# Optimization experiments

Measured on AMD Instinct MI355X. Metric: run time of the kernel, lower is better.

## Reference

```python
import jax, jax.numpy as jnp
import numpy as np

B = 8
RESOLUTIONS = [65, 129, 257, 513, 1025]
NUM_POINTS = [0, 4096, 16384, 65536, 262144]
CLIP_MIN = -1e9
FINAL = 1025          # last resolution (both axes)
B_MIN, B_MAX = -1.0, 1.0
BALANCE = 0.5


def setup_inputs() -> dict:
    key = jax.random.key(0)
    k1, k2, k3, k4 = jax.random.split(key, 4)
    return {
        "w1": jax.random.normal(k1, (2, 256), jnp.float32),
        "b1": jax.random.normal(k2, (256,), jnp.float32),
        "w2": jax.random.normal(k3, (256, 1), jnp.float32),
        "b2": jax.random.normal(k4, (1,), jnp.float32),
    }


def _interp_bilinear_ac(x, H, W):
    """F.interpolate(..., mode='bilinear', align_corners=True). x: [B, C, h, w]."""
    b, c, h, w = x.shape
    ys = jnp.linspace(0.0, h - 1.0, H)
    xs = jnp.linspace(0.0, w - 1.0, W)
    y0 = jnp.floor(ys).astype(jnp.int32)
    y1 = jnp.minimum(y0 + 1, h - 1)
    wy = ys - y0
    x0 = jnp.floor(xs).astype(jnp.int32)
    x1 = jnp.minimum(x0 + 1, w - 1)
    wx = xs - x0
    # interpolate rows, then columns
    top = x[:, :, y0, :] * (1.0 - wy)[None, None, :, None] + x[:, :, y1, :] * wy[None, None, :, None]
    return top[:, :, :, x0] * (1.0 - wx) + top[:, :, :, x1] * wx


def _batch_eval(coords, w1, b1, w2, b2):
    """coords: [B, N, 2] in final-resolution pixel space (align_corners=False mapping).
    Returns occupancy [B, N] (C == 1)."""
    coords2d = coords / FINAL + 0.5 / FINAL                 # normalize to [0, 1]
    p = coords2d * (B_MAX - B_MIN) + B_MIN                  # [B, N, 2] in world coords
    h = jax.nn.relu(jnp.einsum('bnd,dh->bnh', p, w1) + b1)  # [B, N, 256]
    occ = jax.nn.sigmoid(jnp.einsum('bnh,ho->bno', h, w2) + b2)
    return occ[..., 0]


def reference(w1, b1, w2, b2):
    occ = None
    for i, res in enumerate(RESOLUTIONS):
        if i == 0:
            # init_coords: grid of res x res points spanning [0, FINAL-1]
            xs = jnp.linspace(0.0, FINAL - 1.0, res)
            gy, gx = jnp.meshgrid(xs, xs, indexing='ij')          # y rows, x cols
            coords = jnp.stack([gx.ravel(), gy.ravel()], axis=-1)  # [N, 2] (x, y)
            coords = jnp.broadcast_to(coords, (B, res * res, 2))
            o = _batch_eval(coords, w1, b1, w2, b2)               # [B, N]
            occ = o.reshape(B, 1, res, res)                       # [B, C, H, W]
        else:
            occ = _interp_bilinear_ac(occ, res, res)
            npt = NUM_POINTS[i]
            if npt <= 0:
                continue
            # uncertainty = -|occ - balance_value|
            unc = -jnp.abs(occ - BALANCE)                          # [B, 1, H, W]
            flat_unc = unc.reshape(B, res * res)
            scores, idx = jax.lax.top_k(flat_unc, npt)             # [B, npt]
            px = (idx % res).astype(jnp.float32)
            py = (idx // res).astype(jnp.float32)
            stride = (FINAL - 1.0) / (res - 1.0)
            coords = jnp.stack([px, py], axis=-1) * stride         # [B, npt, 2]
            new_vals = _batch_eval(coords, w1, b1, w2, b2)         # [B, npt]
            occ_flat = occ.reshape(B, res * res)
            old_vals = jnp.take_along_axis(occ_flat, idx, axis=1)
            vals = jnp.where(scores >= CLIP_MIN, new_vals, old_vals)
            occ_flat = jax.vmap(lambda o, i2, v: o.at[i2].set(v))(occ_flat, idx, vals)
            occ = occ_flat.reshape(B, 1, res, res)
    return occ
```

## Files before the change

kernel.cpp:

```cpp
#include <hip/hip_runtime.h>
#include <stdint.h>

#define HID 256
#define NMAXPIX (1025 * 1025)
#define NREP 8
#define NSEG 2048
#define SELMAX 2112

#define HISTA_OFF 0
#define HISTB_OFF 16384
#define HISTC_OFF 32768
#define SCAL_OFF  40960
#define TIC_OFF   41024
#define STAGE_U32 43072

#define R1P 65
#define R1  129
#define N1  (129 * 129)
#define NPT1 4096u
#define SEG1 66
#define B1 64
#define NREP1 4

__device__ __forceinline__ uint32_t aload(const uint32_t* p) {
    return __hip_atomic_load(p, __ATOMIC_RELAXED, __HIP_MEMORY_SCOPE_AGENT);
}
__device__ __forceinline__ void astore(uint32_t* p, uint32_t v) {
    __hip_atomic_store(p, v, __ATOMIC_RELAXED, __HIP_MEMORY_SCOPE_AGENT);
}
__device__ __forceinline__ unsigned long long aload64(const unsigned long long* p) {
    return __hip_atomic_load(p, __ATOMIC_RELAXED, __HIP_MEMORY_SCOPE_AGENT);
}
__device__ __forceinline__ void astore64(unsigned long long* p, unsigned long long v) {
    __hip_atomic_store(p, v, __ATOMIC_RELAXED, __HIP_MEMORY_SCOPE_AGENT);
}

__device__ __forceinline__ float mlp_eval4(float wx, float wy,
                                           const float4* __restrict__ w1x,
                                           const float4* __restrict__ w1y,
                                           const float4* __restrict__ vb1,
                                           const float4* __restrict__ vw2, float b2v) {
    const float C0 = (float)(0.5 / 1025.0);
    float px = (wx / 1025.0f + C0) * 2.0f - 1.0f;
    float py = (wy / 1025.0f + C0) * 2.0f - 1.0f;
    float a0 = 0.f, a1 = 0.f, a2 = 0.f, a3 = 0.f;
#pragma unroll 8
    for (int q = 0; q < HID / 4; ++q) {
        float4 a = w1x[q], b = w1y[q], c = vb1[q], d = vw2[q];
        float h0 = px * a.x + py * b.x + c.x;
        float h1 = px * a.y + py * b.y + c.y;
        float h2 = px * a.z + py * b.z + c.z;
        float h3 = px * a.w + py * b.w + c.w;
        h0 = h0 > 0.f ? h0 : 0.f;
        h1 = h1 > 0.f ? h1 : 0.f;
        h2 = h2 > 0.f ? h2 : 0.f;
        h3 = h3 > 0.f ? h3 : 0.f;
        a0 += h0 * d.x;
        a1 += h1 * d.y;
        a2 += h2 * d.z;
        a3 += h3 * d.w;
    }
    float x = ((a0 + a1) + (a2 + a3)) + b2v;
    float r;
    if (x >= 0.f) { r = 1.0f / (1.0f + expf(-x)); }
    else { float e = expf(x); r = e / (1.0f + e); }
    return r;
}

__device__ __forceinline__ uint32_t block_exscan_256(uint32_t v, volatile uint32_t* lds4) {
    int lane = threadIdx.x & 63, w = threadIdx.x >> 6;
    uint32_t inc = v;
#pragma unroll
    for (int d = 1; d < 64; d <<= 1) {
        uint32_t o = (uint32_t)__shfl_up((int)inc, d, 64);
        if (lane >= d) inc += o;
    }
    if (lane == 63) lds4[w] = inc;
    __syncthreads();
    uint32_t woff = 0;
    for (int i = 0; i < w; ++i) woff += lds4[i];
    return woff + inc - v;
}

__device__ void scan_generic(const uint32_t* __restrict__ hist, int NB, int nrep,
                             uint32_t rem_in, uint32_t prefix_in, int shift,
                             uint32_t* outp, uint32_t* outr,
                             volatile uint32_t* lds4, volatile uint32_t* ldspair) {
    int tid = threadIdx.x;
    int C = NB >> 8;
    int b0 = NB - (tid + 1) * C;
    uint32_t cnts[8];
#pragma unroll
    for (int k = 0; k < 8; ++k) cnts[k] = 0;
    for (int rep = 0; rep < nrep; ++rep) {
        const uint4* p = (const uint4*)(hist + (size_t)rep * NB + b0);
#pragma unroll
        for (int g = 0; g < 2; ++g) {
            if (g * 4 < C) {
                uint4 v = p[g];
                cnts[g * 4 + 0] += v.x;
                cnts[g * 4 + 1] += v.y;
                cnts[g * 4 + 2] += v.z;
                cnts[g * 4 + 3] += v.w;
            }
        }
    }
    uint32_t ssum = 0;
    for (int k = 0; k < C; ++k) ssum += cnts[k];
    uint32_t excl = block_exscan_256(ssum, lds4);
    uint32_t run = excl;
    for (int k = 0; k < C; ++k) {
        uint32_t c = cnts[C - 1 - k];
        if (rem_in > run && rem_in <= run + c) {
            ldspair[0] = (prefix_in << shift) | (uint32_t)(b0 + C - 1 - k);
            ldspair[1] = rem_in - run;
        }
        run += c;
    }
    __syncthreads();
    *outp = ldspair[0];
    *outr = ldspair[1];
}

__device__ void scan_atomic(const uint32_t* __restrict__ hist, int NB, int nrep,
                            uint32_t rem_in, uint32_t prefix_in, int shift,
                            uint32_t* outp, uint32_t* outr,
                            volatile uint32_t* lds4, volatile uint32_t* ldspair) {
    int tid = threadIdx.x;
    int C = NB >> 8;
    int b0 = NB - (tid + 1) * C;
    uint32_t cnts[8];
#pragma unroll
    for (int k = 0; k < 8; ++k) cnts[k] = 0;
    for (int rep = 0; rep < nrep; ++rep)
        for (int k = 0; k < C; ++k)
            cnts[k] += aload(&hist[(size_t)rep * NB + b0 + k]);
    uint32_t ssum = 0;
    for (int k = 0; k < C; ++k) ssum += cnts[k];
    uint32_t excl = block_exscan_256(ssum, lds4);
    uint32_t run = excl;
    for (int k = 0; k < C; ++k) {
        uint32_t c = cnts[C - 1 - k];
        if (rem_in > run && rem_in <= run + c) {
            ldspair[0] = (prefix_in << shift) | (uint32_t)(b0 + C - 1 - k);
            ldspair[1] = rem_in - run;
        }
        run += c;
    }
    __syncthreads();
    *outp = ldspair[0];
    *outr = ldspair[1];
}

__device__ __forceinline__ void hist_add(uint32_t* lh, uint32_t bin, bool act, int lane) {
    unsigned long long m = __ballot(act);
    if (m) {
        int leader = __ffsll(m) - 1;
        uint32_t lbin = (uint32_t)__shfl((int)bin, leader, 64);
        unsigned long long smk = __ballot(act && bin == lbin);
        if (smk == m) {
            if (lane == leader) atomicAdd(&lh[lbin], (uint32_t)__popcll(m));
        } else if (act) {
            atomicAdd(&lh[bin], 1u);
        }
    }
}

__device__ __forceinline__ float up2x(const float* __restrict__ in, int rp, int r, int n) {
    int i = n / r, j = n % r;
    int i2 = i >> 1, j2 = j >> 1;
    float v;
    if ((i & 1) == 0) {
        if ((j & 1) == 0) {
            v = in[i2 * rp + j2];
        } else {
            float a = in[i2 * rp + j2], b = in[i2 * rp + j2 + 1];
            v = a * 0.5f + b * 0.5f;
        }
    } else {
        if ((j & 1) == 0) {
            float a = in[i2 * rp + j2], b = in[(i2 + 1) * rp + j2];
            v = a * 0.5f + b * 0.5f;
        } else {
            float a = in[i2 * rp + j2],      c = in[i2 * rp + j2 + 1];
            float b = in[(i2 + 1) * rp + j2], d = in[(i2 + 1) * rp + j2 + 1];
            float t1 = a * 0.5f + b * 0.5f;
            float t2 = c * 0.5f + d * 0.5f;
            v = t1 * 0.5f + t2 * 0.5f;
        }
    }
    return v;
}

__device__ __forceinline__ uint32_t mkkey(float v) {
    float unc = -fabsf(v - 0.5f);
    uint32_t u = __float_as_uint(unc);
    return (u & 0x80000000u) ? ~u : (u | 0x80000000u);
}

__device__ __forceinline__ uint32_t key_of(const float* __restrict__ in, int rp, int r, int n) {
    return mkkey(up2x(in, rp, r, n));
}

__device__ bool wait_ctr(uint32_t* ctr, uint32_t target, volatile uint32_t* sflag) {
    if (threadIdx.x == 0) {
        uint32_t d = aload(ctr);
        int sp = 0;
        while (d < target && sp < 20000) {
            __builtin_amdgcn_s_sleep(4);
            d = aload(ctr);
            ++sp;
        }
        *sflag = (d >= target) ? 1u : 0u;
    }
    __syncthreads();
    return *sflag != 0;
}

__global__ __launch_bounds__(256) void k_eval0z(const float* __restrict__ w1, const float* __restrict__ b1,
                                                const float* __restrict__ w2, const float* __restrict__ b2,
                                                float* __restrict__ occ, uint32_t* __restrict__ zbuf, int zcount) {
    __shared__ alignas(16) float sw1[2 * HID];
    __shared__ alignas(16) float sb1[HID];
    __shared__ alignas(16) float sw2[HID];
    int tid = threadIdx.x;
    for (int i = tid; i < 2 * HID; i += 256) sw1[i] = w1[i];
    sb1[tid] = b1[tid];
    sw2[tid] = w2[tid];
    __syncthreads();
    int gtid = blockIdx.x * 256 + tid;
    int nthreads = gridDim.x * 256;
    for (int i = gtid; i < zcount; i += nthreads) zbuf[i] = 0;
    for (int n = gtid; n < 65 * 65; n += nthreads) {
        int i = n / 65, j = n % 65;
        occ[n] = mlp_eval4(16.0f * (float)j, 16.0f * (float)i,
                           (const float4*)sw1, (const float4*)(sw1 + HID),
                           (const float4*)sb1, (const float4*)sw2, b2[0]);
    }
}

__global__ __launch_bounds__(256) void k_s1all(const float* __restrict__ in,
                                               float* __restrict__ outg,
                                               uint32_t* __restrict__ keys,
                                               uint32_t* __restrict__ sm,
                                               const float* __restrict__ w1, const float* __restrict__ b1,
                                               const float* __restrict__ w2, const float* __restrict__ b2) {
    __shared__ alignas(16) float sw1[2 * HID];
    __shared__ alignas(16) float sb1[HID];
    __shared__ alignas(16) float sw2[HID];
    __shared__ alignas(16) uint32_t lh[2048];
    __shared__ uint32_t selidx[SELMAX];
    __shared__ uint32_t selcnt;
    __shared__ uint32_t lds4[4];
    __shared__ uint32_t ldspair[2];
    __shared__ uint32_t sflag;

    uint32_t* histA = sm + HISTA_OFF;
    uint32_t* histB = sm + HISTB_OFF;
    uint32_t* histC = sm + HISTC_OFF;
    uint32_t* scal  = sm + SCAL_OFF;
    uint32_t* tic   = sm + TIC_OFF;

    const int tid = threadIdx.x, lane = tid & 63, w = tid >> 6;
    for (int i = tid; i < 2 * HID; i += 256) sw1[i] = w1[i];
    sb1[tid] = b1[tid];
    sw2[tid] = w2[tid];
    if (tid == 0) selcnt = 0;
    for (int k = tid; k < 2048; k += 256) lh[k] = 0;
    __syncthreads();

    for (int n0 = blockIdx.x * 256; n0 < N1; n0 += B1 * 256) {
        int n = n0 + tid;
        bool act = n < N1;
        uint32_t key = 0;
        if (act) {
            float v = up2x(in, R1P, R1, n);
            outg[n] = v;
            key = mkkey(v);
            astore(&keys[n], key);
        }
        hist_add(lh, key >> 21, act, lane);
    }
    __syncthreads();
    {
        uint32_t* rep = histA + (size_t)(blockIdx.x & (NREP1 - 1)) * 2048;
        for (int k = tid; k < 2048; k += 256) { uint32_t c = lh[k]; if (c) atomicAdd(&rep[k], c); }
    }
    __syncthreads();
    if (tid == 0) __hip_atomic_fetch_add(&scal[8], 1u, __ATOMIC_RELAXED, __HIP_MEMORY_SCOPE_AGENT);

    uint32_t pfx1, rem1;
    if (wait_ctr(&scal[8], B1, &sflag)) {
        scan_atomic(histA, 2048, NREP1, NPT1, 0u, 0, &pfx1, &rem1, lds4, ldspair);
    } else {
        for (int k = tid; k < 2048; k += 256) lh[k] = 0;
        __syncthreads();
        for (int n0 = 0; n0 < N1; n0 += 256) {
            int n = n0 + tid; bool act = n < N1;
            uint32_t key = act ? key_of(in, R1P, R1, n) : 0u;
            hist_add(lh, key >> 21, act, lane);
        }
        __syncthreads();
        scan_generic(lh, 2048, 1, NPT1, 0u, 0, &pfx1, &rem1, lds4, ldspair);
    }

    for (int k = tid; k < 2048; k += 256) lh[k] = 0;
    __syncthreads();
    for (int n0 = blockIdx.x * 256; n0 < N1; n0 += B1 * 256) {
        int n = n0 + tid;
        bool act = n < N1;
        uint32_t key = act ? aload(&keys[n]) : 0u;
        bool flt = act && ((key >> 21) == pfx1);
        hist_add(lh, (key >> 10) & 0x7FFu, flt, lane);
    }
    __syncthreads();
    {
        uint32_t* rep = histB + (size_t)(blockIdx.x & (NREP1 - 1)) * 2048;
        for (int k = tid; k < 2048; k += 256) { uint32_t c = lh[k]; if (c) atomicAdd(&rep[k], c); }
    }
    __syncthreads();
    if (tid == 0) __hip_atomic_fetch_add(&scal[9], 1u, __ATOMIC_RELAXED, __HIP_MEMORY_SCOPE_AGENT);

    uint32_t pfx2, rem2;
    if (wait_ctr(&scal[9], B1, &sflag)) {
        scan_atomic(histB, 2048, NREP1, rem1, pfx1, 11, &pfx2, &rem2, lds4, ldspair);
    } else {
        for (int k = tid; k < 2048; k += 256) lh[k] = 0;
        __syncthreads();
        for (int n0 = 0; n0 < N1; n0 += 256) {
            int n = n0 + tid; bool act = n < N1;
            uint32_t key = act ? key_of(in, R1P, R1, n) : 0u;
            bool flt = act && ((key >> 21) == pfx1);
            hist_add(lh, (key >> 10) & 0x7FFu, flt, lane);
        }
        __syncthreads();
        scan_generic(lh, 2048, 1, rem1, pfx1, 11, &pfx2, &rem2, lds4, ldspair);
    }

    for (int k = tid; k < 2048; k += 256) lh[k] = 0;
    __syncthreads();
    for (int n0 = blockIdx.x * 256; n0 < N1; n0 += B1 * 256) {
        int n = n0 + tid;
        bool act = n < N1;
        uint32_t key = act ? aload(&keys[n]) : 0u;
        bool flt = act && ((key >> 10) == pfx2);
        hist_add(lh, key & 0x3FFu, flt, lane);
    }
    __syncthreads();
    {
        uint32_t* rep = histC + (size_t)(blockIdx.x & (NREP1 - 1)) * 1024;
        for (int k = tid; k < 1024; k += 256) { uint32_t c = lh[k]; if (c) atomicAdd(&rep[k], c); }
    }
    __syncthreads();
    if (tid == 0) __hip_atomic_fetch_add(&scal[10], 1u, __ATOMIC_RELAXED, __HIP_MEMORY_SCOPE_AGENT);

    uint32_t K, t;
    if (wait_ctr(&scal[10], B1, &sflag)) {
        scan_atomic(histC, 1024, NREP1, rem2, pfx2, 10, &K, &t, lds4, ldspair);
    } else {
        for (int k = tid; k < 2048; k += 256) lh[k] = 0;
        __syncthreads();
        for (int n0 = 0; n0 < N1; n0 += 256) {
            int n = n0 + tid; bool act = n < N1;
            uint32_t key = act ? key_of(in, R1P, R1, n) : 0u;
            bool flt = act && ((key >> 10) == pfx2);
            hist_add(lh, key & 0x3FFu, flt, lane);
        }
        __syncthreads();
        scan_generic(lh, 1024, 1, rem2, pfx2, 10, &K, &t, lds4, ldspair);
    }

    int wv = blockIdx.x * 4 + w;
    int s0 = wv * SEG1;
    int s1e = s0 + SEG1; if (s1e > N1) s1e = N1;
    uint32_t tcnt = 0;
    for (int base = s0; base < s1e; base += 64) {
        int n = base + lane;
        if (n < s1e) tcnt += (aload(&keys[n]) == K) ? 1u : 0u;
    }
#pragma unroll
    for (int d = 32; d; d >>= 1) tcnt += (uint32_t)__shfl_down((int)tcnt, d, 64);
    if (lane == 0) astore(&tic[wv], tcnt);
    __syncthreads();
    if (tid == 0) __hip_atomic_fetch_add(&scal[11], 1u, __ATOMIC_RELAXED, __HIP_MEMORY_SCOPE_AGENT);

    uint32_t tp = 0;
    if (wait_ctr(&scal[11], B1, &sflag)) {
        for (int i = lane; i < wv; i += 64) tp += aload(&tic[i]);
    } else {
        for (int i = lane; i < wv; i += 64) {
            int a0 = i * SEG1, a1 = a0 + SEG1; if (a1 > N1) a1 = N1;
            uint32_t c = 0;
            for (int n2 = a0; n2 < a1; ++n2) c += (key_of(in, R1P, R1, n2) == K) ? 1u : 0u;
            tp += c;
        }
    }
#pragma unroll
    for (int d = 32; d; d >>= 1) tp += (uint32_t)__shfl_down((int)tp, d, 64);
    tp = (uint32_t)__shfl((int)tp, 0, 64);

    uint32_t tie_run = tp;
    unsigned long long lowmask = (lane == 63) ? ~0ull >> 1 : ((1ull << lane) - 1ull);
    for (int base = s0; base < s1e; base += 64) {
        int n = base + lane;
        bool inb = n < s1e;
        uint32_t key = inb ? aload(&keys[n]) : 0u;
        bool gt = inb && (key > K);
        bool tie = inb && (key == K);
        unsigned long long tm = __ballot(tie);
        uint32_t trank = tie_run + (uint32_t)__popcll(tm & lowmask);
        bool sel = gt || (tie && trank < t);
        unsigned long long smk = __ballot(sel);
        if (smk) {
            int leader = __ffsll(smk) - 1;
            uint32_t wbase = 0;
            if (lane == leader) wbase = atomicAdd(&selcnt, (uint32_t)__popcll(smk));
            wbase = (uint32_t)__shfl((int)wbase, leader, 64);
            if (sel) selidx[wbase + (uint32_t)__popcll(smk & lowmask)] = (uint32_t)n;
        }
        tie_run += (uint32_t)__popcll(tm);
    }
    __syncthreads();

    uint32_t cnt = selcnt;
    float vb2 = b2[0];
    for (uint32_t i = tid; i < cnt; i += 256) {
        int n = (int)selidx[i];
        int ii = n / R1, jj = n % R1;
        float rr = mlp_eval4(8.0f * (float)jj, 8.0f * (float)ii,
                             (const float4*)sw1, (const float4*)(sw1 + HID),
                             (const float4*)sb1, (const float4*)sw2, vb2);
        outg[n] = rr;
    }
}

__global__ __launch_bounds__(256) void k_upkey(const float* __restrict__ in, int rp,
                                               float* __restrict__ outg, int r, int nb, int bstride,
                                               uint32_t* __restrict__ keys,
                                               uint32_t* __restrict__ histA) {
    __shared__ uint32_t hist[2048];
    int tid = threadIdx.x;
    for (int k = tid; k < 2048; k += 256) hist[k] = 0;
    __syncthreads();
    int N = r * r;
    int lane = tid & 63;
    int gstride = gridDim.x * 256;
    for (int n0 = blockIdx.x * 256; n0 < N; n0 += gstride) {
        int n = n0 + tid;
        bool act = n < N;
        uint32_t key = 0;
        if (act) {
            float v = up2x(in, rp, r, n);
            for (int k = 0; k < nb; ++k) outg[(size_t)k * bstride + n] = v;
            key = mkkey(v);
            keys[n] = key;
        }
        hist_add(hist, key >> 21, act, lane);
    }
    __syncthreads();
    uint32_t* myrep = histA + (size_t)(blockIdx.x & (NREP - 1)) * 2048;
    for (int k = tid; k < 2048; k += 256) {
        uint32_t c = hist[k];
        if (c) atomicAdd(&myrep[k], c);
    }
}

__global__ __launch_bounds__(256) void k_histmid(const uint32_t* __restrict__ keys, int N,
                                                 const uint32_t* __restrict__ prevHist,
                                                 uint32_t* __restrict__ scal,
                                                 int useNpt, uint32_t npt, int scalInIdx, int shift,
                                                 int scalOutIdx,
                                                 int fshift, int bshift, uint32_t bmask,
                                                 uint32_t* __restrict__ outHist, int NBout) {
    __shared__ uint32_t lh[2048];
    __shared__ uint32_t lds4[4];
    __shared__ uint32_t ldspair[2];
    int tid = threadIdx.x, lane = tid & 63;
    uint32_t rem_in = useNpt ? npt : scal[scalInIdx + 1];
    uint32_t pfx_in = useNpt ? 0u  : scal[scalInIdx];
    uint32_t pfx, rem;
    scan_generic(prevHist, 2048, NREP, rem_in, pfx_in, shift, &pfx, &rem, lds4, ldspair);
    if (blockIdx.x == 0 && tid == 0) { scal[scalOutIdx] = pfx; scal[scalOutIdx + 1] = rem; }
    for (int k = tid; k < 2048; k += 256) lh[k] = 0;
    __syncthreads();
    int gstride = gridDim.x * 256;
    for (int base = blockIdx.x * 256; base < N; base += gstride) {
        int n = base + tid;
        bool inb = n < N;
        uint32_t key = inb ? keys[n] : 0u;
        bool flt = inb && ((key >> fshift) == pfx);
        uint32_t bin = (key >> bshift) & bmask;
        hist_add(lh, bin, flt, lane);
    }
    __syncthreads();
    uint32_t* myrep = outHist + (size_t)(blockIdx.x & (NREP - 1)) * NBout;
    for (int k = tid; k < NBout; k += 256) {
        uint32_t c = lh[k];
        if (c) atomicAdd(&myrep[k], c);
    }
}

__global__ __launch_bounds__(256, 2) void k_segselc(
        const uint32_t* __restrict__ keys, int N, int seglen,
        const uint32_t* __restrict__ histC,
        const uint32_t* __restrict__ scal,
        unsigned long long* __restrict__ tic64,
        uint32_t* __restrict__ selbuf) {
    __shared__ uint32_t lds4[4];
    __shared__ uint32_t ldspair[2];
    __shared__ uint32_t wtc[4], wgc[4];
    __shared__ uint32_t s_excl_t, s_excl_g;
    int tid = threadIdx.x, lane = tid & 63, w = tid >> 6;
    if (tid == 0) { s_excl_t = 0; s_excl_g = 0; }

    uint32_t rem2 = scal[3], pfx2 = scal[2];
    uint32_t K, t;
    scan_generic(histC, 1024, NREP, rem2, pfx2, 10, &K, &t, lds4, ldspair);

    int wv = blockIdx.x * 4 + w;
    int s0 = wv * seglen;
    int s1 = s0 + seglen; if (s1 > N) s1 = N;
    uint32_t tcnt = 0, gcnt2 = 0;
    for (int base = s0; base < s1; base += 64) {
        int n = base + lane;
        if (n < s1) {
            uint32_t key = keys[n];
            tcnt += (key == K) ? 1u : 0u;
            gcnt2 += (key > K) ? 1u : 0u;
        }
    }
#pragma unroll
    for (int d = 32; d; d >>= 1) {
        tcnt += (uint32_t)__shfl_down((int)tcnt, d, 64);
        gcnt2 += (uint32_t)__shfl_down((int)gcnt2, d, 64);
    }
    if (lane == 0) { wtc[w] = tcnt; wgc[w] = gcnt2; }
    __syncthreads();
    uint32_t agg_t = wtc[0] + wtc[1] + wtc[2] + wtc[3];
    uint32_t agg_g = wgc[0] + wgc[1] + wgc[2] + wgc[3];
    uint32_t intra_t = 0, intra_g = 0;
    for (int i = 0; i < w; ++i) { intra_t += wtc[i]; intra_g += wgc[i]; }

    if (tid == 0) {
        unsigned long long pay = ((unsigned long long)agg_t << 24) | (unsigned long long)agg_g;
        unsigned long long st = (blockIdx.x == 0) ? ((2ull << 62) | pay) : ((1ull << 62) | pay);
        astore64(&tic64[blockIdx.x], st);
    }
    if (blockIdx.x > 0 && w == 0) {
        uint32_t excl_t = 0, excl_g = 0;
        int b = (int)blockIdx.x - 1;
        for (;;) {
            int mine = b - lane;
            bool active = (mine >= 0);
            unsigned long long f = 0;
            if (active) {
                f = aload64(&tic64[mine]);
                int spins = 0;
                while ((f >> 62) == 0ull && spins < 1000) {
                    __builtin_amdgcn_s_sleep(2);
                    f = aload64(&tic64[mine]);
                    ++spins;
                }
                if ((f >> 62) == 0ull) {
                    int ms0 = mine * 4 * seglen;
                    int ms1 = ms0 + 4 * seglen; if (ms1 > N) ms1 = N;
                    uint32_t ct = 0, cg = 0;
                    for (int n2 = ms0; n2 < ms1; ++n2) {
                        uint32_t key = keys[n2];
                        ct += (key == K) ? 1u : 0u;
                        cg += (key > K) ? 1u : 0u;
                    }
                    f = (1ull << 62) | ((unsigned long long)ct << 24) | (unsigned long long)cg;
                }
            }
            unsigned long long incm = __ballot(active && (f >> 62) == 2ull);
            uint32_t vt, vg;
            bool done = (incm != 0ull);
            if (done) {
                int l2 = __ffsll(incm) - 1;
                vt = (lane <= l2) ? (uint32_t)((f >> 24) & 0xFFFFFFull) : 0u;
                vg = (lane <= l2) ? (uint32_t)(f & 0xFFFFFFull) : 0u;
            } else {
                vt = active ? (uint32_t)((f >> 24) & 0xFFFFFFull) : 0u;
                vg = active ? (uint32_t)(f & 0xFFFFFFull) : 0u;
            }
#pragma unroll
            for (int d = 32; d; d >>= 1) {
                vt += (uint32_t)__shfl_down((int)vt, d, 64);
                vg += (uint32_t)__shfl_down((int)vg, d, 64);
            }
            vt = (uint32_t)__shfl((int)vt, 0, 64);
            vg = (uint32_t)__shfl((int)vg, 0, 64);
            excl_t += vt;
            excl_g += vg;
            if (done) break;
            if (b < 64) break;
            b -= 64;
        }
        if (lane == 0) {
            unsigned long long pay = ((unsigned long long)(excl_t + agg_t) << 24)
                                   | (unsigned long long)(excl_g + agg_g);
            astore64(&tic64[blockIdx.x], (2ull << 62) | pay);
            s_excl_t = excl_t;
            s_excl_g = excl_g;
        }
    }
    __syncthreads();
    uint32_t tie_run = s_excl_t + intra_t;
    uint32_t gt_run  = s_excl_g + intra_g;

    unsigned long long lowmask = (lane == 63) ? ~0ull >> 1 : ((1ull << lane) - 1ull);
    for (int base = s0; base < s1; base += 64) {
        int n = base + lane;
        bool inb = n < s1;
        uint32_t key = inb ? keys[n] : 0u;
        bool gt = inb && (key > K);
        bool tie = inb && (key == K);
        unsigned long long tm = __ballot(tie);
        unsigned long long gm = __ballot(gt);
        uint32_t tie_before = tie_run + (uint32_t)__popcll(tm & lowmask);
        uint32_t gt_before  = gt_run + (uint32_t)__popcll(gm & lowmask);
        if (gt) {
            uint32_t tb = tie_before < t ? tie_before : t;
            selbuf[gt_before + tb] = (uint32_t)n;
        } else if (tie && tie_before < t) {
            selbuf[gt_before + tie_before] = (uint32_t)n;
        }
        tie_run += (uint32_t)__popcll(tm);
        gt_run  += (uint32_t)__popcll(gm);
    }
}

__global__ __launch_bounds__(256) void k_evalsel(const uint32_t* __restrict__ selbuf, int npt,
                                                 int r, float stride,
                                                 float* __restrict__ occ, int nb, int bstride,
                                                 const float* __restrict__ w1, const float* __restrict__ b1,
                                                 const float* __restrict__ w2, const float* __restrict__ b2) {
    __shared__ alignas(16) float sw1[2 * HID];
    __shared__ alignas(16) float sb1[HID];
    __shared__ alignas(16) float sw2[HID];
    int tid = threadIdx.x;
    for (int i = tid; i < 2 * HID; i += 256) sw1[i] = w1[i];
    sb1[tid] = b1[tid];
    sw2[tid] = w2[tid];
    __syncthreads();
    float vb2 = b2[0];
    const float4* w1x = (const float4*)sw1;
    const float4* w1y = (const float4*)(sw1 + HID);
    const float4* vb1 = (const float4*)sb1;
    const float4* vw2 = (const float4*)sw2;
    const float C0 = (float)(0.5 / 1025.0);
    int gs2 = gridDim.x * 512;
    for (int bb = blockIdx.x * 512; bb < npt; bb += gs2) {
        int i0 = bb + tid, i1 = bb + tid + 256;
        bool v0 = i0 < npt, v1 = i1 < npt;
        int nA = v0 ? (int)selbuf[i0] : 0;
        int nB = v1 ? (int)selbuf[i1] : 0;
        int iA = nA / r, jA = nA % r;
        int iB = nB / r, jB = nB % r;
        float pxA = ((stride * (float)jA) / 1025.0f + C0) * 2.0f - 1.0f;
        float pyA = ((stride * (float)iA) / 1025.0f + C0) * 2.0f - 1.0f;
        float pxB = ((stride * (float)jB) / 1025.0f + C0) * 2.0f - 1.0f;
        float pyB = ((stride * (float)iB) / 1025.0f + C0) * 2.0f - 1.0f;
        float4 A0 = {0, 0, 0, 0}, A1 = {0, 0, 0, 0};
#pragma unroll 4
        for (int q = 0; q < HID / 4; ++q) {
            float4 a = w1x[q], b = w1y[q], c = vb1[q], d = vw2[q];
            {
                float h0 = pxA * a.x + pyA * b.x + c.x;
                float h1 = pxA * a.y + pyA * b.y + c.y;
                float h2 = pxA * a.z + pyA * b.z + c.z;
                float h3 = pxA * a.w + pyA * b.w + c.w;
                h0 = h0 > 0.f ? h0 : 0.f;
                h1 = h1 > 0.f ? h1 : 0.f;
                h2 = h2 > 0.f ? h2 : 0.f;
                h3 = h3 > 0.f ? h3 : 0.f;
                A0.x += h0 * d.x; A0.y += h1 * d.y;
                A0.z += h2 * d.z; A0.w += h3 * d.w;
            }
            {
                float h0 = pxB * a.x + pyB * b.x + c.x;
                float h1 = pxB * a.y + pyB * b.y + c.y;
                float h2 = pxB * a.z + pyB * b.z + c.z;
                float h3 = pxB * a.w + pyB * b.w + c.w;
                h0 = h0 > 0.f ? h0 : 0.f;
                h1 = h1 > 0.f ? h1 : 0.f;
                h2 = h2 > 0.f ? h2 : 0.f;
                h3 = h3 > 0.f ? h3 : 0.f;
                A1.x += h0 * d.x; A1.y += h1 * d.y;
                A1.z += h2 * d.z; A1.w += h3 * d.w;
            }
        }
        if (v0) {
            float x = ((A0.x + A0.y) + (A0.z + A0.w)) + vb2;
            float rr;
            if (x >= 0.f) { rr = 1.0f / (1.0f + expf(-x)); }
            else { float e = expf(x); rr = e / (1.0f + e); }
            for (int k = 0; k < nb; ++k) occ[(size_t)k * bstride + nA] = rr;
        }
        if (v1) {
            float x = ((A1.x + A1.y) + (A1.z + A1.w)) + vb2;
            float rr;
            if (x >= 0.f) { rr = 1.0f / (1.0f + expf(-x)); }
            else { float e = expf(x); rr = e / (1.0f + e); }
            for (int k = 0; k < nb; ++k) occ[(size_t)k * bstride + nB] = rr;
        }
    }
}

__global__ __launch_bounds__(256) void k_bcast(const float* __restrict__ src, float* __restrict__ dst, int N) {
    int q = blockIdx.x * 256 + threadIdx.x;
    int n = q * 4;
    if (n + 3 < N) {
        float4 v = *(const float4*)(src + n);
#pragma unroll
        for (int k = 0; k < 8; ++k) *(float4*)(dst + (size_t)k * N + n) = v;
    } else if (n < N) {
        for (int m = n; m < N; ++m) {
            float v = src[m];
#pragma unroll
            for (int k = 0; k < 8; ++k) dst[(size_t)k * N + m] = v;
        }
    }
}

extern "C" void kernel_launch(void* const* d_in, const int* in_sizes, int n_in,
                              void* d_out, int out_size, void* d_ws, size_t ws_size,
                              hipStream_t stream) {
    const float* w1 = (const float*)d_in[0];
    const float* b1 = (const float*)d_in[1];
    const float* w2 = (const float*)d_in[2];
    const float* b2 = (const float*)d_in[3];
    float* out = (float*)d_out;

    const size_t A = (((size_t)NMAXPIX * 4) + 255) & ~(size_t)255;
    const size_t SMALL_BYTES = (size_t)4 * STAGE_U32 * 4;
    const size_t SELB_BYTES = ((size_t)262144 * 4 + 255) & ~(size_t)255;
    const size_t need = 3 * A + SMALL_BYTES + SELB_BYTES;

    int fused8 = (ws_size >= need);
    char* base = fused8 ? (char*)d_ws : (char*)d_out;
    float* buf0 = (float*)(base);
    float* buf1 = (float*)(base + A);
    uint32_t* keys = (uint32_t*)(base + 2 * A);
    uint32_t* smallb = (uint32_t*)(base + 3 * A);
    uint32_t* selbuf = (uint32_t*)(base + 3 * A + SMALL_BYTES);

    k_eval0z<<<dim3(512), dim3(256), 0, stream>>>(w1, b1, w2, b2, buf0, smallb, 4 * STAGE_U32);

    k_s1all<<<dim3(B1), dim3(256), 0, stream>>>(buf0, buf1, keys, smallb, w1, b1, w2, b2);

    const int resA[5] = {65, 129, 257, 513, 1025};
    const int nptA[5] = {0, 4096, 16384, 65536, 262144};
    float* cur = buf1;
    float* nxt = buf0;
    for (int s = 2; s < 5; ++s) {
        int rp = resA[s - 1], r = resA[s];
        int N = r * r;
        uint32_t npt = (uint32_t)nptA[s];
        uint32_t* sm    = smallb + (size_t)(s - 1) * STAGE_U32;
        uint32_t* histA = sm + HISTA_OFF;
        uint32_t* histB = sm + HISTB_OFF;
        uint32_t* histC = sm + HISTC_OFF;
        uint32_t* scal  = sm + SCAL_OFF;
        uint32_t* tic   = sm + TIC_OFF;
        int nb1 = (N + 255) / 256;
        int nbu = nb1 < 1024 ? nb1 : 1024;
        int seglen = (N + NSEG - 1) / NSEG;
        float stride = 1024.0f / (float)(r - 1);

        int last = (s == 4);
        float* stage_out = (last && fused8) ? out : nxt;
        int nb = (last && fused8) ? 8 : 1;
        int bstride = (last && fused8) ? NMAXPIX : 0;

        int nbe = (int)((npt + 511) / 512); if (nbe > 512) nbe = 512;

        k_upkey<<<dim3(nbu), dim3(256), 0, stream>>>(cur, rp, stage_out, r, nb, bstride, keys, histA);
        k_histmid<<<dim3(512), dim3(256), 0, stream>>>(keys, N, histA, scal, 1, npt, 0, 0,
                                                       0, 21, 10, 0x7FFu, histB, 2048);
        k_histmid<<<dim3(512), dim3(256), 0, stream>>>(keys, N, histB, scal, 0, 0u, 0, 11,
                                                       2, 10, 0, 0x3FFu, histC, 1024);
        k_segselc<<<dim3(NSEG / 4), dim3(256), 0, stream>>>(keys, N, seglen, histC, scal,
                                                            (unsigned long long*)tic, selbuf);
        k_evalsel<<<dim3(nbe), dim3(256), 0, stream>>>(selbuf, (int)npt, r, stride,
                                                       stage_out, nb, bstride, w1, b1, w2, b2);
        if (!(last && fused8)) { float* tmp = cur; cur = nxt; nxt = tmp; }
    }
    if (!fused8) {
        k_bcast<<<dim3(((NMAXPIX + 3) / 4 + 255) / 256), dim3(256), 0, stream>>>(cur, out, NMAXPIX);
    }
}
```

Measured before the change: 229.6 us.

## Fuse upsample, radix-select and segment compaction into one persistent kernel for mid stages

```diff
diff --git a/kernel.cpp b/kernel.cpp
--- a/kernel.cpp
+++ b/kernel.cpp
@@ -5,7 +5,6 @@
 #define NMAXPIX (1025 * 1025)
 #define NREP 8
 #define NSEG 2048
-#define SELMAX 2112
 
 #define HISTA_OFF 0
 #define HISTB_OFF 16384
@@ -249,7 +248,7 @@
     __shared__ alignas(16) float sb1[HID];
     __shared__ alignas(16) float sw2[HID];
     __shared__ alignas(16) uint32_t lh[2048];
-    __shared__ uint32_t selidx[SELMAX];
+    __shared__ uint32_t selidx[2112];
     __shared__ uint32_t selcnt;
     __shared__ uint32_t lds4[4];
     __shared__ uint32_t ldspair[2];
@@ -431,6 +430,196 @@
                              (const float4*)sw1, (const float4*)(sw1 + HID),
                              (const float4*)sb1, (const float4*)sw2, vb2);
         outg[n] = rr;
+    }
+}
+
+__global__ __launch_bounds__(256) void k_ssel(const float* __restrict__ in, int rp, int r,
+                                              int N, uint32_t npt, int seglen,
+                                              float* __restrict__ outg,
+                                              uint32_t* __restrict__ keys,
+                                              uint32_t* __restrict__ sm,
+                                              uint32_t* __restrict__ selbuf) {
+    __shared__ alignas(16) uint32_t lh[2048];
+    __shared__ uint32_t lds4[4];
+    __shared__ uint32_t ldspair[2];
+    __shared__ uint32_t sflag;
+
+    uint32_t* histA = sm + HISTA_OFF;
+    uint32_t* histB = sm + HISTB_OFF;
+    uint32_t* histC = sm + HISTC_OFF;
+    uint32_t* scal  = sm + SCAL_OFF;
+    uint32_t* tict  = sm + TIC_OFF;
+    uint32_t* ticg  = sm + TIC_OFF + 256;
+
+    const int tid = threadIdx.x, lane = tid & 63, w = tid >> 6;
+    for (int k = tid; k < 2048; k += 256) lh[k] = 0;
+    __syncthreads();
+
+    for (int n0 = blockIdx.x * 256; n0 < N; n0 += B1 * 256) {
+        int n = n0 + tid;
+        bool act = n < N;
+        uint32_t key = 0;
+        if (act) {
+            float v = up2x(in, rp, r, n);
+            outg[n] = v;
+            key = mkkey(v);
+            astore(&keys[n], key);
+        }
+        hist_add(lh, key >> 21, act, lane);
+    }
+    __syncthreads();
+    {
+        uint32_t* rep = histA + (size_t)(blockIdx.x & (NREP1 - 1)) * 2048;
+        for (int k = tid; k < 2048; k += 256) { uint32_t c = lh[k]; if (c) atomicAdd(&rep[k], c); }
+    }
+    __syncthreads();
+    if (tid == 0) __hip_atomic_fetch_add(&scal[8], 1u, __ATOMIC_RELAXED, __HIP_MEMORY_SCOPE_AGENT);
+
+    uint32_t pfx1, rem1;
+    if (wait_ctr(&scal[8], B1, &sflag)) {
+        scan_atomic(histA, 2048, NREP1, npt, 0u, 0, &pfx1, &rem1, lds4, ldspair);
+    } else {
+        for (int k = tid; k < 2048; k += 256) lh[k] = 0;
+        __syncthreads();
+        for (int n0 = 0; n0 < N; n0 += 256) {
+            int n = n0 + tid; bool act = n < N;
+            uint32_t key = act ? key_of(in, rp, r, n) : 0u;
+            hist_add(lh, key >> 21, act, lane);
+        }
+        __syncthreads();
+        scan_generic(lh, 2048, 1, npt, 0u, 0, &pfx1, &rem1, lds4, ldspair);
+    }
+
+    for (int k = tid; k < 2048; k += 256) lh[k] = 0;
+    __syncthreads();
+    for (int n0 = blockIdx.x * 256; n0 < N; n0 += B1 * 256) {
+        int n = n0 + tid;
+        bool act = n < N;
+        uint32_t key = act ? aload(&keys[n]) : 0u;
+        bool flt = act && ((key >> 21) == pfx1);
+        hist_add(lh, (key >> 10) & 0x7FFu, flt, lane);
+    }
+    __syncthreads();
+    {
+        uint32_t* rep = histB + (size_t)(blockIdx.x & (NREP1 - 1)) * 2048;
+        for (int k = tid; k < 2048; k += 256) { uint32_t c = lh[k]; if (c) atomicAdd(&rep[k], c); }
+    }
+    __syncthreads();
+    if (tid == 0) __hip_atomic_fetch_add(&scal[9], 1u, __ATOMIC_RELAXED, __HIP_MEMORY_SCOPE_AGENT);
+
+    uint32_t pfx2, rem2;
+    if (wait_ctr(&scal[9], B1, &sflag)) {
+        scan_atomic(histB, 2048, NREP1, rem1, pfx1, 11, &pfx2, &rem2, lds4, ldspair);
+    } else {
+        for (int k = tid; k < 2048; k += 256) lh[k] = 0;
+        __syncthreads();
+        for (int n0 = 0; n0 < N; n0 += 256) {
+            int n = n0 + tid; bool act = n < N;
+            uint32_t key = act ? key_of(in, rp, r, n) : 0u;
+            bool flt = act && ((key >> 21) == pfx1);
+            hist_add(lh, (key >> 10) & 0x7FFu, flt, lane);
+        }
+        __syncthreads();
+        scan_generic(lh, 2048, 1, rem1, pfx1, 11, &pfx2, &rem2, lds4, ldspair);
+    }
+
+    for (int k = tid; k < 2048; k += 256) lh[k] = 0;
+    __syncthreads();
+    for (int n0 = blockIdx.x * 256; n0 < N; n0 += B1 * 256) {
+        int n = n0 + tid;
+        bool act = n < N;
+        uint32_t key = act ? aload(&keys[n]) : 0u;
+        bool flt = act && ((key >> 10) == pfx2);
+        hist_add(lh, key & 0x3FFu, flt, lane);
+    }
+    __syncthreads();
+    {
+        uint32_t* rep = histC + (size_t)(blockIdx.x & (NREP1 - 1)) * 1024;
+        for (int k = tid; k < 1024; k += 256) { uint32_t c = lh[k]; if (c) atomicAdd(&rep[k], c); }
+    }
+    __syncthreads();
+    if (tid == 0) __hip_atomic_fetch_add(&scal[10], 1u, __ATOMIC_RELAXED, __HIP_MEMORY_SCOPE_AGENT);
+
+    uint32_t K, t;
+    if (wait_ctr(&scal[10], B1, &sflag)) {
+        scan_atomic(histC, 1024, NREP1, rem2, pfx2, 10, &K, &t, lds4, ldspair);
+    } else {
+        for (int k = tid; k < 2048; k += 256) lh[k] = 0;
+        __syncthreads();
+        for (int n0 = 0; n0 < N; n0 += 256) {
+            int n = n0 + tid; bool act = n < N;
+            uint32_t key = act ? key_of(in, rp, r, n) : 0u;
+            bool flt = act && ((key >> 10) == pfx2);
+            hist_add(lh, key & 0x3FFu, flt, lane);
+        }
+        __syncthreads();
+        scan_generic(lh, 1024, 1, rem2, pfx2, 10, &K, &t, lds4, ldspair);
+    }
+
+    int wv = blockIdx.x * 4 + w;
+    int s0 = wv * seglen;
+    int s1e = s0 + seglen; if (s1e > N) s1e = N;
+    uint32_t tcnt = 0, gcnt = 0;
+    for (int base = s0; base < s1e; base += 64) {
+        int n = base + lane;
+        if (n < s1e) {
+            uint32_t key = aload(&keys[n]);
+            tcnt += (key == K) ? 1u : 0u;
+            gcnt += (key > K) ? 1u : 0u;
+        }
+    }
+#pragma unroll
+    for (int d = 32; d; d >>= 1) {
+        tcnt += (uint32_t)__shfl_down((int)tcnt, d, 64);
+        gcnt += (uint32_t)__shfl_down((int)gcnt, d, 64);
+    }
+    if (lane == 0) { astore(&tict[wv], tcnt); astore(&ticg[wv], gcnt); }
+    __syncthreads();
+    if (tid == 0) __hip_atomic_fetch_add(&scal[11], 1u, __ATOMIC_RELAXED, __HIP_MEMORY_SCOPE_AGENT);
+
+    uint32_t tp = 0, gp = 0;
+    if (wait_ctr(&scal[11], B1, &sflag)) {
+        for (int i = lane; i < wv; i += 64) { tp += aload(&tict[i]); gp += aload(&ticg[i]); }
+    } else {
+        for (int i = lane; i < wv; i += 64) {
+            int a0 = i * seglen, a1 = a0 + seglen; if (a1 > N) a1 = N;
+            uint32_t ct = 0, cg = 0;
+            for (int n2 = a0; n2 < a1; ++n2) {
+                uint32_t key = key_of(in, rp, r, n2);
+                ct += (key == K) ? 1u : 0u;
+                cg += (key > K) ? 1u : 0u;
+            }
+            tp += ct; gp += cg;
+        }
+    }
+#pragma unroll
+    for (int d = 32; d; d >>= 1) {
+        tp += (uint32_t)__shfl_down((int)tp, d, 64);
+        gp += (uint32_t)__shfl_down((int)gp, d, 64);
+    }
+    tp = (uint32_t)__shfl((int)tp, 0, 64);
+    gp = (uint32_t)__shfl((int)gp, 0, 64);
+
+    uint32_t tie_run = tp, gt_run = gp;
+    unsigned long long lowmask = (lane == 63) ? ~0ull >> 1 : ((1ull << lane) - 1ull);
+    for (int base = s0; base < s1e; base += 64) {
+        int n = base + lane;
+        bool inb = n < s1e;
+        uint32_t key = inb ? aload(&keys[n]) : 0u;
+        bool gt = inb && (key > K);
+        bool tie = inb && (key == K);
+        unsigned long long tm = __ballot(tie);
+        unsigned long long gm = __ballot(gt);
+        uint32_t tie_before = tie_run + (uint32_t)__popcll(tm & lowmask);
+        uint32_t gt_before  = gt_run + (uint32_t)__popcll(gm & lowmask);
+        if (gt) {
+            uint32_t tb = tie_before < t ? tie_before : t;
+            astore(&selbuf[gt_before + tb], (uint32_t)n);
+        } else if (tie && tie_before < t) {
+            astore(&selbuf[gt_before + tie_before], (uint32_t)n);
+        }
+        tie_run += (uint32_t)__popcll(tm);
+        gt_run  += (uint32_t)__popcll(gm);
     }
 }
 
@@ -754,7 +943,25 @@
     const int nptA[5] = {0, 4096, 16384, 65536, 262144};
     float* cur = buf1;
     float* nxt = buf0;
-    for (int s = 2; s < 5; ++s) {
+
+    for (int s = 2; s < 4; ++s) {
+        int rp = resA[s - 1], r = resA[s];
+        int N = r * r;
+        uint32_t npt = (uint32_t)nptA[s];
+        uint32_t* sm = smallb + (size_t)(s - 1) * STAGE_U32;
+        int seglen = (N + 255) / 256;
+        float stride = 1024.0f / (float)(r - 1);
+        int nbe = (int)((npt + 511) / 512); if (nbe > 512) nbe = 512;
+
+        k_ssel<<<dim3(B1), dim3(256), 0, stream>>>(cur, rp, r, N, npt, seglen,
+                                                   nxt, keys, sm, selbuf);
+        k_evalsel<<<dim3(nbe), dim3(256), 0, stream>>>(selbuf, (int)npt, r, stride,
+                                                       nxt, 1, 0, w1, b1, w2, b2);
+        float* tmp = cur; cur = nxt; nxt = tmp;
+    }
+
+    {
+        const int s = 4;
         int rp = resA[s - 1], r = resA[s];
         int N = r * r;
         uint32_t npt = (uint32_t)nptA[s];
@@ -769,11 +976,9 @@
         int seglen = (N + NSEG - 1) / NSEG;
         float stride = 1024.0f / (float)(r - 1);
 
-        int last = (s == 4);
-        float* stage_out = (last && fused8) ? out : nxt;
-        int nb = (last && fused8) ? 8 : 1;
-        int bstride = (last && fused8) ? NMAXPIX : 0;
-
+        float* stage_out = fused8 ? out : nxt;
+        int nb = fused8 ? 8 : 1;
+        int bstride = fused8 ? NMAXPIX : 0;
         int nbe = (int)((npt + 511) / 512); if (nbe > 512) nbe = 512;
 
         k_upkey<<<dim3(nbu), dim3(256), 0, stream>>>(cur, rp, stage_out, r, nb, bstride, keys, histA);
@@ -785,7 +990,7 @@
                                                             (unsigned long long*)tic, selbuf);
         k_evalsel<<<dim3(nbe), dim3(256), 0, stream>>>(selbuf, (int)npt, r, stride,
                                                        stage_out, nb, bstride, w1, b1, w2, b2);
-        if (!(last && fused8)) { float* tmp = cur; cur = nxt; nxt = tmp; }
+        if (!fused8) { float* tmp = cur; cur = nxt; nxt = tmp; }
     }
     if (!fused8) {
         k_bcast<<<dim3(((NMAXPIX + 3) / 4 + 255) / 256), dim3(256), 0, stream>>>(cur, out, NMAXPIX);
```

New measurement: 273.9 us. 19.3% more time.
